# Kernel tuning notes

Hardware: AMD Instinct MI355X
Metric: run time of the kernel (lower is better)

## Reference

```python
import jax, jax.numpy as jnp
import numpy as np

D_MODEL = 1024
D_STATE = 16
D_CONV = 4
EXPAND = 2
D_INNER = EXPAND * D_MODEL          # 2048
DT_RANK = (D_MODEL + 15) // 16      # 64
B, L = 4, 2048


def setup_inputs() -> dict:
    key = jax.random.key(0)
    ks = jax.random.split(key, 10)
    s = 0.02
    x = jax.random.normal(ks[0], (B, L, D_MODEL), dtype=jnp.float32)
    # weights stored (in, out) so y = x @ W
    W_in = jax.random.normal(ks[1], (D_MODEL, 2 * D_INNER), dtype=jnp.float32) * s
    conv_w = jax.random.normal(ks[2], (D_INNER, D_CONV), dtype=jnp.float32) * 0.2
    conv_b = jnp.zeros((D_INNER,), dtype=jnp.float32)
    W_xproj = jax.random.normal(ks[3], (D_INNER, DT_RANK + 2 * D_STATE), dtype=jnp.float32) * s
    W_dt = jax.random.normal(ks[4], (DT_RANK, D_INNER), dtype=jnp.float32) * s
    b_dt = jax.random.uniform(ks[5], (D_INNER,), dtype=jnp.float32, minval=-4.0, maxval=-2.0)
    # S4D real init: A = -exp(A_log), A_log = log(1..d_state)
    A_log = jnp.log(jnp.broadcast_to(jnp.arange(1, D_STATE + 1, dtype=jnp.float32), (D_INNER, D_STATE)))
    Dp = jnp.ones((D_INNER,), dtype=jnp.float32)
    W_out = jax.random.normal(ks[6], (D_INNER, D_MODEL), dtype=jnp.float32) * s
    return {"x": x, "W_in": W_in, "conv_w": conv_w, "conv_b": conv_b,
            "W_xproj": W_xproj, "W_dt": W_dt, "b_dt": b_dt,
            "A_log": A_log, "Dp": Dp, "W_out": W_out}


def _causal_depthwise_conv(u, conv_w, conv_b):
    # u: (B, L, D_INNER); depthwise causal conv, kernel D_CONV
    uc = jnp.transpose(u, (0, 2, 1))                      # (B, D, L)
    k = conv_w[:, None, :]                                # (D, 1, K)
    y = jax.lax.conv_general_dilated(
        uc, k, window_strides=(1,), padding=[(D_CONV - 1, 0)],
        feature_group_count=D_INNER,
        dimension_numbers=('NCH', 'OIH', 'NCH'))
    y = y + conv_b[None, :, None]
    return jnp.transpose(y, (0, 2, 1))                    # (B, L, D)


def _selective_scan(u, delta, A, Bm, Cm, Dp):
    # u, delta: (B, L, d); A: (d, n); Bm, Cm: (B, L, n)
    def step(h, inp):
        u_t, dt_t, B_t, C_t = inp                         # (B,d),(B,d),(B,n),(B,n)
        dA = jnp.exp(dt_t[..., None] * A)                 # (B, d, n)
        h = h * dA + (dt_t * u_t)[..., None] * B_t[:, None, :]
        y = jnp.einsum('bdn,bn->bd', h, C_t)
        return h, y

    h0 = jnp.zeros((u.shape[0], u.shape[2], A.shape[1]), dtype=u.dtype)
    xs = (jnp.swapaxes(u, 0, 1), jnp.swapaxes(delta, 0, 1),
          jnp.swapaxes(Bm, 0, 1), jnp.swapaxes(Cm, 0, 1))
    _, ys = jax.lax.scan(step, h0, xs)
    y = jnp.swapaxes(ys, 0, 1)                            # (B, L, d)
    return y + u * Dp


def reference(x, W_in, conv_w, conv_b, W_xproj, W_dt, b_dt, A_log, Dp, W_out):
    xz = x @ W_in                                         # (B, L, 2*D_INNER)
    u, z = jnp.split(xz, 2, axis=-1)
    u = jax.nn.silu(_causal_depthwise_conv(u, conv_w, conv_b))
    proj = u @ W_xproj                                    # (B, L, DT_RANK + 2*D_STATE)
    dt_r = proj[..., :DT_RANK]
    Bm = proj[..., DT_RANK:DT_RANK + D_STATE]
    Cm = proj[..., DT_RANK + D_STATE:]
    delta = jax.nn.softplus(dt_r @ W_dt + b_dt)           # (B, L, D_INNER)
    A = -jnp.exp(A_log)                                   # (D_INNER, D_STATE)
    y = _selective_scan(u, delta, A, Bm, Cm, Dp)
    y = y * jax.nn.silu(z)
    return y @ W_out
```

## Files before the change

### kernel.cpp

```cpp
#include <hip/hip_runtime.h>
#include <hip/hip_bf16.h>
#include <math.h>

#define MTOK   8192
#define LSEQ   2048
#define NBATCH 4
#define DMODEL 1024
#define DINNER 2048
#define DSTATE 16
#define DTRANK 64
#define NXZ    4096
#define CHUNK  64
#define NCH    32
#define NPROJ  (MTOK * 96)
#define SPLITK 8

typedef _Float16 f16;
using f16x8 = __attribute__((ext_vector_type(8))) _Float16;
using f16x4 = __attribute__((ext_vector_type(4))) _Float16;
using f32x4 = __attribute__((ext_vector_type(4))) float;

__device__ __forceinline__ float silu_f(float x) { return x / (1.f + __expf(-x)); }

__device__ __forceinline__ void gload_lds16(const void* g, void* l) {
    __builtin_amdgcn_global_load_lds(
        (const __attribute__((address_space(1))) void*)g,
        (__attribute__((address_space(3))) void*)l, 16, 0, 0);
}

__global__ __launch_bounds__(256)
void cvt_f2h(const float* __restrict__ in, f16* __restrict__ out, int n4)
{
    const int i = blockIdx.x * 256 + threadIdx.x;
    if (i >= n4) return;
    const float4 v = ((const float4*)in)[i];
    f16x4 o;
    o[0] = (f16)v.x; o[1] = (f16)v.y; o[2] = (f16)v.z; o[3] = (f16)v.w;
    ((f16x4*)out)[i] = o;
}

__global__ __launch_bounds__(256)
void tcvt(const float* __restrict__ in, f16* __restrict__ out, int R, int C)
{
    __shared__ float t[32][33];
    const int c0 = blockIdx.x * 32, r0 = blockIdx.y * 32;
    const int tx = threadIdx.x & 31, ty = threadIdx.x >> 5;
    #pragma unroll
    for (int j = 0; j < 4; ++j)
        t[ty + 8 * j][tx] = in[(size_t)(r0 + ty + 8 * j) * C + c0 + tx];
    __syncthreads();
    #pragma unroll
    for (int j = 0; j < 4; ++j)
        out[(size_t)(c0 + ty + 8 * j) * R + r0 + tx] = (f16)t[tx][ty + 8 * j];
}

template<int EPI, typename OUT_T>
__global__ __launch_bounds__(256)
void hgemm128(const f16* __restrict__ A, int lda,
              const f16* __restrict__ Bt, int ldb,
              OUT_T* __restrict__ C, int ldc,
              int K, const float* __restrict__ bias,
              OUT_T* __restrict__ C2, int splitcol)
{
    __shared__ __align__(16) f16 As[2][128 * 32];
    __shared__ __align__(16) f16 Bs[2][128 * 32];

    const int tid  = threadIdx.x;
    const int lane = tid & 63, wave = tid >> 6;
    const int wr = wave >> 1, wc = wave & 1;
    const int row0 = blockIdx.x * 128;
    int col0 = blockIdx.y * 128;

    const int lrow = lane >> 2;
    const int lcol = ((lane & 3) ^ ((lane >> 3) & 3)) * 8;
    const f16* Agw = A  + (size_t)(row0 + wave * 32 + lrow) * lda + lcol;
    const f16* Bgw = Bt + (size_t)(col0 + wave * 32 + lrow) * ldb + lcol;
    const int ldsbase = (wave * 32) * 32;

    const int frow = lane & 15;
    const int fk   = (((lane >> 4) ^ ((frow >> 1) & 3))) * 8;
    const int nt = K / 32;

    f32x4 acc[4][4] = {};

    #pragma unroll
    for (int r = 0; r < 2; ++r) {
        gload_lds16(Agw + (size_t)r * 16 * lda, &As[0][ldsbase + r * 16 * 32]);
        gload_lds16(Bgw + (size_t)r * 16 * ldb, &Bs[0][ldsbase + r * 16 * 32]);
    }

    int cur = 0;
    for (int kt = 0; kt < nt; ++kt) {
        __syncthreads();
        if (kt + 1 < nt) {
            const int k0 = (kt + 1) * 32;
            #pragma unroll
            for (int r = 0; r < 2; ++r) {
                gload_lds16(Agw + (size_t)r * 16 * lda + k0, &As[cur ^ 1][ldsbase + r * 16 * 32]);
                gload_lds16(Bgw + (size_t)r * 16 * ldb + k0, &Bs[cur ^ 1][ldsbase + r * 16 * 32]);
            }
        }
        f16x8 af[4], bf[4];
        #pragma unroll
        for (int m = 0; m < 4; ++m)
            af[m] = *(const f16x8*)&As[cur][(wr * 64 + m * 16 + frow) * 32 + fk];
        #pragma unroll
        for (int n = 0; n < 4; ++n)
            bf[n] = *(const f16x8*)&Bs[cur][(wc * 64 + n * 16 + frow) * 32 + fk];
        #pragma unroll
        for (int m = 0; m < 4; ++m)
            #pragma unroll
            for (int n = 0; n < 4; ++n)
                acc[m][n] = __builtin_amdgcn_mfma_f32_16x16x32_f16(af[m], bf[n], acc[m][n], 0, 0, 0);
        cur ^= 1;
    }

    OUT_T* Cw = C;
    if (C2 != nullptr && col0 >= splitcol) { Cw = C2; col0 -= splitcol; }

    const int rbase = row0 + wr * 64 + (lane >> 4) * 4;
    const int cbase = col0 + wc * 64 + (lane & 15);
    #pragma unroll
    for (int m = 0; m < 4; ++m) {
        #pragma unroll
        for (int n = 0; n < 4; ++n) {
            const int col = cbase + n * 16;
            #pragma unroll
            for (int r = 0; r < 4; ++r) {
                const int row = rbase + m * 16 + r;
                float tv = acc[m][n][r];
                if (EPI == 1) {
                    tv += bias[col];
                    tv = (tv > 20.f) ? tv : __logf(1.f + __expf(tv));
                }
                Cw[(size_t)row * ldc + col] = (OUT_T)tv;
            }
        }
    }
}

__global__ __launch_bounds__(256)
void hgemm_n96(const f16* __restrict__ A,
               const f16* __restrict__ Bt,
               float* __restrict__ part)
{
    __shared__ __align__(16) f16 As[128][40];
    __shared__ __align__(16) f16 Bs[96][40];

    const int tid = threadIdx.x, lane = tid & 63, wave = tid >> 6;
    const int row0 = blockIdx.x * 128;
    const int sk = blockIdx.y;
    const int kbase = sk * (DINNER / SPLITK);

    const int srow = tid >> 1, skoff = (tid & 1) * 16;
    const f16* Ag = A  + (size_t)(row0 + srow) * DINNER + kbase + skoff;
    const f16* Bg = Bt + (size_t)srow * DINNER + kbase + skoff;

    const int frow = lane & 15, fk = (lane >> 4) * 8;

    f32x4 acc[2][6] = {};

    for (int kk = 0; kk < DINNER / SPLITK; kk += 32) {
        const f16x8 a0 = *(const f16x8*)(Ag + kk);
        const f16x8 a1 = *(const f16x8*)(Ag + kk + 8);
        f16x8 b0 = {}, b1 = {};
        if (tid < 192) { b0 = *(const f16x8*)(Bg + kk); b1 = *(const f16x8*)(Bg + kk + 8); }
        __syncthreads();
        *(f16x8*)&As[srow][skoff]     = a0;
        *(f16x8*)&As[srow][skoff + 8] = a1;
        if (tid < 192) {
            *(f16x8*)&Bs[srow][skoff]     = b0;
            *(f16x8*)&Bs[srow][skoff + 8] = b1;
        }
        __syncthreads();

        f16x8 af[2], bf[6];
        #pragma unroll
        for (int m = 0; m < 2; ++m)
            af[m] = *(const f16x8*)&As[wave * 32 + m * 16 + frow][fk];
        #pragma unroll
        for (int n = 0; n < 6; ++n)
            bf[n] = *(const f16x8*)&Bs[n * 16 + frow][fk];
        #pragma unroll
        for (int m = 0; m < 2; ++m)
            #pragma unroll
            for (int n = 0; n < 6; ++n)
                acc[m][n] = __builtin_amdgcn_mfma_f32_16x16x32_f16(af[m], bf[n], acc[m][n], 0, 0, 0);
    }

    #pragma unroll
    for (int m = 0; m < 2; ++m)
        #pragma unroll
        for (int n = 0; n < 6; ++n) {
            const int col = n * 16 + (lane & 15);
            #pragma unroll
            for (int r = 0; r < 4; ++r) {
                const int row = row0 + wave * 32 + m * 16 + (lane >> 4) * 4 + r;
                part[((size_t)sk * MTOK + row) * 96 + col] = acc[m][n][r];
            }
        }
}

__global__ __launch_bounds__(256)
void reduce3(const float* __restrict__ part, float* __restrict__ proj,
             f16* __restrict__ projh)
{
    const int e = blockIdx.x * 256 + threadIdx.x;
    float s = 0.f;
    #pragma unroll
    for (int i = 0; i < SPLITK; ++i) s += part[(size_t)i * NPROJ + e];
    proj[e]  = s;
    projh[e] = (f16)s;
}

__global__ __launch_bounds__(256)
void conv_silu_kernel(const f16* __restrict__ uph,
                      const float* __restrict__ cw, const float* __restrict__ cb,
                      f16* __restrict__ uh)
{
    const int mt  = blockIdx.x;
    const int ml0 = mt * 8;
    const int l0  = ml0 & (LSEQ - 1);
    const int d   = threadIdx.x * 8;

    float w[8][4];
    #pragma unroll
    for (int c = 0; c < 8; ++c) {
        const float4 wv = *(const float4*)(cw + (size_t)(d + c) * 4);
        w[c][0] = wv.x; w[c][1] = wv.y; w[c][2] = wv.z; w[c][3] = wv.w;
    }
    float bias[8];
    {
        const float4 b0 = *(const float4*)(cb + d);
        const float4 b1 = *(const float4*)(cb + d + 4);
        bias[0] = b0.x; bias[1] = b0.y; bias[2] = b0.z; bias[3] = b0.w;
        bias[4] = b1.x; bias[5] = b1.y; bias[6] = b1.z; bias[7] = b1.w;
    }

    f16x8 r[11];
    if (l0 != 0) {
        #pragma unroll
        for (int i = 0; i < 11; ++i)
            r[i] = *(const f16x8*)(uph + (size_t)(ml0 - 3 + i) * DINNER + d);
    } else {
        r[0] = f16x8{}; r[1] = f16x8{}; r[2] = f16x8{};
        #pragma unroll
        for (int i = 3; i < 11; ++i)
            r[i] = *(const f16x8*)(uph + (size_t)(ml0 - 3 + i) * DINNER + d);
    }

    #pragma unroll
    for (int i = 0; i < 8; ++i) {
        f16x8 o;
        #pragma unroll
        for (int c = 0; c < 8; ++c) {
            float a = bias[c];
            #pragma unroll
            for (int j = 0; j < 4; ++j)
                a = fmaf((float)r[i + j][c], w[c][j], a);
            o[c] = (f16)silu_f(a);
        }
        *(f16x8*)(uh + (size_t)(ml0 + i) * DINNER + d) = o;
    }
}

__device__ __forceinline__ bool load_A(const float* __restrict__ A_log, int d,
                                       float* Av)
{
    #pragma unroll
    for (int n = 0; n < DSTATE; ++n)
        Av[n] = -__expf(A_log[(size_t)d * DSTATE + n]);
    bool p = true;
    #pragma unroll
    for (int n = 1; n < DSTATE; ++n) {
        const float r = Av[n] / Av[0];
        if (fabsf(r - (float)(n + 1)) > 1e-3f) p = false;
    }
    return p;
}

__global__ __launch_bounds__(256)
void scan_pass1(const f16* __restrict__ uh,
                const f16* __restrict__ deltah,
                const float* __restrict__ proj,
                const float* __restrict__ A_log,
                float* __restrict__ Sbuf, float* __restrict__ sumdt)
{
    const int d = blockIdx.x * 256 + threadIdx.x;
    const int c = blockIdx.y;
    const int b = blockIdx.z;

    float Av[DSTATE];
    const bool pw = load_A(A_log, d, Av);
    const float Av0 = Av[0];

    const float* projb = proj + ((size_t)b * LSEQ + (size_t)c * CHUNK) * 96 + 64;

    float S[DSTATE];
    #pragma unroll
    for (int n = 0; n < DSTATE; ++n) S[n] = 0.f;
    float sdt = 0.f;

    const size_t tok0 = (size_t)b * LSEQ + (size_t)c * CHUNK;
    if (pw) {
        for (int l = 0; l < CHUNK; ++l) {
            const float* pr = projb + (size_t)l * 96;
            const float dt = (float)deltah[(tok0 + l) * DINNER + d];
            const float uu = (float)uh[(tok0 + l) * DINNER + d];
            sdt += dt;
            const float du = dt * uu;
            const float p1 = __expf(dt * Av0);
            const float p2 = p1 * p1;
            const float p3 = p2 * p1;
            const float p4 = p2 * p2;
            float m = 1.f;
            #pragma unroll
            for (int g = 0; g < 4; ++g) {
                const f32x4 bb = *(const f32x4*)(pr + g * 4);
                S[g*4+0] = fmaf(S[g*4+0], m * p1, du * bb[0]);
                S[g*4+1] = fmaf(S[g*4+1], m * p2, du * bb[1]);
                S[g*4+2] = fmaf(S[g*4+2], m * p3, du * bb[2]);
                S[g*4+3] = fmaf(S[g*4+3], m * p4, du * bb[3]);
                m *= p4;
            }
        }
    } else {
        for (int l = 0; l < CHUNK; ++l) {
            const float* pr = projb + (size_t)l * 96;
            const float dt = (float)deltah[(tok0 + l) * DINNER + d];
            const float uu = (float)uh[(tok0 + l) * DINNER + d];
            sdt += dt;
            const float du = dt * uu;
            #pragma unroll
            for (int n = 0; n < DSTATE; ++n)
                S[n] = fmaf(S[n], __expf(dt * Av[n]), du * pr[n]);
        }
    }

    const size_t base = (size_t)b * NCH + c;
    #pragma unroll
    for (int n = 0; n < DSTATE; ++n)
        Sbuf[(base * DSTATE + n) * DINNER + d] = S[n];
    sumdt[base * DINNER + d] = sdt;
}

__global__ __launch_bounds__(256)
void scan_pass2(const float* __restrict__ A_log,
                const float* __restrict__ sumdt,
                float* __restrict__ Sbuf)
{
    const int d = blockIdx.x * 256 + threadIdx.x;
    const int b = blockIdx.y;

    float Av[DSTATE];
    const bool pw = load_A(A_log, d, Av);
    const float Av0 = Av[0];

    float h[DSTATE];
    #pragma unroll
    for (int n = 0; n < DSTATE; ++n) h[n] = 0.f;

    for (int c = 0; c < NCH; ++c) {
        const size_t base = (size_t)b * NCH + c;
        const float sdt = sumdt[base * DINNER + d];
        if (pw) {
            const float p1 = __expf(sdt * Av0);
            const float p2 = p1 * p1;
            const float p3 = p2 * p1;
            const float p4 = p2 * p2;
            float m = 1.f;
            #pragma unroll
            for (int g = 0; g < 4; ++g) {
                const float pj[4] = {p1, p2, p3, p4};
                #pragma unroll
                for (int j = 0; j < 4; ++j) {
                    const int n = g * 4 + j;
                    const size_t idx = (base * DSTATE + n) * DINNER + d;
                    const float tmp = Sbuf[idx];
                    Sbuf[idx] = h[n];
                    h[n] = fmaf(h[n], m * pj[j], tmp);
                }
                m *= p4;
            }
        } else {
            #pragma unroll
            for (int n = 0; n < DSTATE; ++n) {
                const size_t idx = (base * DSTATE + n) * DINNER + d;
                const float tmp = Sbuf[idx];
                Sbuf[idx] = h[n];
                h[n] = fmaf(h[n], __expf(sdt * Av[n]), tmp);
            }
        }
    }
}

__global__ __launch_bounds__(256)
void scan_pass3(const f16* __restrict__ uh,
                const f16* __restrict__ deltah,
                const f16* __restrict__ zh,
                const float* __restrict__ proj,
                const float* __restrict__ A_log,
                const float* __restrict__ Dp,
                const float* __restrict__ Sbuf,
                f16* __restrict__ ygh)
{
    const int d = blockIdx.x * 256 + threadIdx.x;
    const int c = blockIdx.y;
    const int b = blockIdx.z;

    float Av[DSTATE];
    const bool pw = load_A(A_log, d, Av);
    const float Av0 = Av[0];

    float h[DSTATE];
    const size_t base = (size_t)b * NCH + c;
    #pragma unroll
    for (int n = 0; n < DSTATE; ++n)
        h[n] = Sbuf[(base * DSTATE + n) * DINNER + d];

    const float Dval = Dp[d];
    const float* projb = proj + ((size_t)b * LSEQ + (size_t)c * CHUNK) * 96 + 64;

    const size_t tok0 = (size_t)b * LSEQ + (size_t)c * CHUNK;
    for (int l = 0; l < CHUNK; ++l) {
        const float* pr = projb + (size_t)l * 96;
        const size_t tok = tok0 + l;
        const float dt = (float)deltah[tok * DINNER + d];
        const float uu = (float)uh[tok * DINNER + d];
        const float zz = (float)zh[tok * DINNER + d];
        const float du = dt * uu;
        float y = 0.f;
        if (pw) {
            const float p1 = __expf(dt * Av0);
            const float p2 = p1 * p1;
            const float p3 = p2 * p1;
            const float p4 = p2 * p2;
            float m = 1.f;
            #pragma unroll
            for (int g = 0; g < 4; ++g) {
                const f32x4 bb = *(const f32x4*)(pr + g * 4);
                const f32x4 cc = *(const f32x4*)(pr + 16 + g * 4);
                h[g*4+0] = fmaf(h[g*4+0], m * p1, du * bb[0]);
                h[g*4+1] = fmaf(h[g*4+1], m * p2, du * bb[1]);
                h[g*4+2] = fmaf(h[g*4+2], m * p3, du * bb[2]);
                h[g*4+3] = fmaf(h[g*4+3], m * p4, du * bb[3]);
                y = fmaf(h[g*4+0], cc[0], y);
                y = fmaf(h[g*4+1], cc[1], y);
                y = fmaf(h[g*4+2], cc[2], y);
                y = fmaf(h[g*4+3], cc[3], y);
                m *= p4;
            }
        } else {
            #pragma unroll
            for (int n = 0; n < DSTATE; ++n) {
                h[n] = fmaf(h[n], __expf(dt * Av[n]), du * pr[n]);
                y = fmaf(h[n], pr[16 + n], y);
            }
        }
        const float yt = fmaf(uu, Dval, y);
        ygh[tok * DINNER + d] = (f16)(yt * silu_f(zz));
    }
}

extern "C" void kernel_launch(void* const* d_in, const int* in_sizes, int n_in,
                              void* d_out, int out_size, void* d_ws, size_t ws_size,
                              hipStream_t stream)
{
    const float* x     = (const float*)d_in[0];
    const float* W_in  = (const float*)d_in[1];
    const float* cw    = (const float*)d_in[2];
    const float* cb    = (const float*)d_in[3];
    const float* W_xp  = (const float*)d_in[4];
    const float* W_dt  = (const float*)d_in[5];
    const float* b_dt  = (const float*)d_in[6];
    const float* A_log = (const float*)d_in[7];
    const float* Dp    = (const float*)d_in[8];
    const float* W_out = (const float*)d_in[9];
    float* out = (float*)d_out;

    float* updelta = (float*)d_ws;
    f16*   zh      = (f16*)(updelta + (size_t)MTOK * DINNER);
    f16*   uh      = zh + (size_t)MTOK * DINNER;
    float* proj    = (float*)(uh + (size_t)MTOK * DINNER);
    f16*   projh   = (f16*)(proj + NPROJ);
    float* Sbuf    = (float*)(projh + NPROJ);
    float* sumdt   = Sbuf + (size_t)NBATCH * NCH * DSTATE * DINNER;
    f16*   WxpT    = (f16*)(sumdt + (size_t)NBATCH * NCH * DINNER);
    f16*   WdtT    = WxpT + (size_t)96 * DINNER;
    f16*   WoutT   = WdtT + (size_t)DINNER * DTRANK;
    f16*   big     = WoutT + (size_t)DMODEL * DINNER;
    f16*   WinT    = big;
    float* part3   = (float*)(big + (size_t)NXZ * DMODEL);
    f16*   ygh     = big;
    f16*   xh      = uh;
    f16*   uph     = (f16*)updelta;
    f16*   deltah  = (f16*)updelta;

    cvt_f2h<<<(MTOK * DMODEL / 4 + 255) / 256, 256, 0, stream>>>(x, xh, MTOK * DMODEL / 4);
    tcvt<<<dim3(NXZ / 32, DMODEL / 32), 256, 0, stream>>>(W_in, WinT, DMODEL, NXZ);

    hgemm128<0, f16><<<dim3(64, 32), 256, 0, stream>>>(
        xh, DMODEL, WinT, DMODEL, uph, DINNER, DMODEL, nullptr, zh, DINNER);

    conv_silu_kernel<<<MTOK / 8, 256, 0, stream>>>(uph, cw, cb, uh);

    tcvt<<<dim3(96 / 32, DINNER / 32), 256, 0, stream>>>(W_xp, WxpT, DINNER, 96);
    hgemm_n96<<<dim3(64, SPLITK), 256, 0, stream>>>(uh, WxpT, part3);
    reduce3<<<NPROJ / 256, 256, 0, stream>>>(part3, proj, projh);

    tcvt<<<dim3(DINNER / 32, DTRANK / 32), 256, 0, stream>>>(W_dt, WdtT, DTRANK, DINNER);
    hgemm128<1, f16><<<dim3(64, 16), 256, 0, stream>>>(
        projh, 96, WdtT, DTRANK, deltah, DINNER, DTRANK, b_dt, nullptr, 0);

    scan_pass1<<<dim3(DINNER / 256, NCH, NBATCH), 256, 0, stream>>>(
        uh, deltah, proj, A_log, Sbuf, sumdt);
    scan_pass2<<<dim3(DINNER / 256, NBATCH), 256, 0, stream>>>(A_log, sumdt, Sbuf);
    scan_pass3<<<dim3(DINNER / 256, NCH, NBATCH), 256, 0, stream>>>(
        uh, deltah, zh, proj, A_log, Dp, Sbuf, ygh);

    tcvt<<<dim3(DMODEL / 32, DINNER / 32), 256, 0, stream>>>(W_out, WoutT, DINNER, DMODEL);
    hgemm128<0, float><<<dim3(64, 8), 256, 0, stream>>>(
        ygh, DINNER, WoutT, DINNER, out, DMODEL, DINNER, nullptr, nullptr, 0);
}
```

Baseline: 328.6 us.

## Replace in-projection GEMM with 256x256-tile, 8-wave pipelined MFMA kernel

Adds a new 512-thread GEMM with 256x256 output tiles, K-step 64, and swizzled LDS layout. Global-to-LDS loads are issued in half-tile pieces interleaved with the MFMA phases, with explicit waitcnt, barriers and setprio. It is used only for the large x@W_in projection. The goal is more data reuse per tile and better overlap of loads with compute. The cost is only 512 blocks at one block per CU and heavy register use from 32 accumulators per thread.

```diff
diff --git a/kernel.cpp b/kernel.cpp
--- a/kernel.cpp
+++ b/kernel.cpp
@@ -52,6 +52,115 @@
     #pragma unroll
     for (int j = 0; j < 4; ++j)
         out[(size_t)(c0 + ty + 8 * j) * R + r0 + tx] = (f16)t[tx][ty + 8 * j];
+}
+
+__global__ __launch_bounds__(512, 1)
+void hgemm256p(const f16* __restrict__ A, int lda,
+               const f16* __restrict__ Bt, int ldb,
+               f16* __restrict__ C, int ldc,
+               int K, f16* __restrict__ C2, int splitcol)
+{
+    __shared__ __align__(16) f16 SA[2][16384];
+    __shared__ __align__(16) f16 SB[2][16384];
+
+    const int tid  = threadIdx.x;
+    const int lane = tid & 63, w = tid >> 6;
+    const int wr = w >> 2, wc = w & 3;
+    const int row0 = blockIdx.x * 256;
+    int col0 = blockIdx.y * 256;
+
+    const int frow = lane & 15;
+    const int nt = K / 64;
+
+    auto issue_half = [&](int q) {
+        const int t = q >> 2, j = q & 3, buf = t & 1, k0 = t * 64;
+        const bool isA = (j >= 2);
+        const int hh = j & 1;
+        const f16* base = isA ? (A  + (size_t)(row0 + hh * 128) * lda + k0)
+                              : (Bt + (size_t)(col0 + hh * 128) * ldb + k0);
+        const int ld = isA ? lda : ldb;
+        f16* dst = (isA ? &SA[buf][0] : &SB[buf][0]) + hh * 8192;
+        #pragma unroll
+        for (int r2 = 0; r2 < 2; ++r2) {
+            const int ch = r2 * 512 + tid;
+            const int grow = ch >> 3;
+            const int gcol = (((ch & 7) * 16) ^ (((ch >> 5) & 1) << 5)) >> 1;
+            gload_lds16(base + (size_t)grow * ld + gcol, dst + ch * 8);
+        }
+    };
+
+    int next = 0;
+    for (; next < 6 && next < 4 * nt; ++next) issue_half(next);
+    asm volatile("s_waitcnt vmcnt(4)" ::: "memory");
+    asm volatile("s_barrier" ::: "memory");
+
+    f32x4 acc[8][4] = {};
+
+    for (int t = 0; t < nt; ++t) {
+        const int buf = t & 1;
+        const char* Ab = (const char*)&SA[buf][0];
+        const char* Bb = (const char*)&SB[buf][0];
+        f16x8 bf[4][2];
+        #pragma unroll
+        for (int p = 0; p < 4; ++p) {
+            f16x8 af[2][2];
+            if (p == 0) {
+                #pragma unroll
+                for (int n = 0; n < 4; ++n)
+                    #pragma unroll
+                    for (int ks = 0; ks < 2; ++ks) {
+                        const int R = wc * 64 + n * 16 + frow;
+                        const int off = R * 128 +
+                            ((ks * 64 + (lane >> 4) * 16) ^ (((R >> 2) & 1) << 5));
+                        bf[n][ks] = *(const f16x8*)(Bb + off);
+                    }
+            }
+            #pragma unroll
+            for (int i = 0; i < 2; ++i)
+                #pragma unroll
+                for (int ks = 0; ks < 2; ++ks) {
+                    const int R = wr * 128 + (2 * p + i) * 16 + frow;
+                    const int off = R * 128 +
+                        ((ks * 64 + (lane >> 4) * 16) ^ (((R >> 2) & 1) << 5));
+                    af[i][ks] = *(const f16x8*)(Ab + off);
+                }
+            if (next < 4 * nt) issue_half(next++);
+            asm volatile("s_barrier" ::: "memory");
+            asm volatile("s_waitcnt lgkmcnt(0)" ::: "memory");
+            __builtin_amdgcn_sched_barrier(0);
+            __builtin_amdgcn_s_setprio(1);
+            #pragma unroll
+            for (int i = 0; i < 2; ++i)
+                #pragma unroll
+                for (int n = 0; n < 4; ++n)
+                    #pragma unroll
+                    for (int ks = 0; ks < 2; ++ks)
+                        acc[2 * p + i][n] = __builtin_amdgcn_mfma_f32_16x16x32_f16(
+                            af[i][ks], bf[n][ks], acc[2 * p + i][n], 0, 0, 0);
+            __builtin_amdgcn_s_setprio(0);
+            if (p == 3 && t + 1 < nt) {
+                if (next >= 4 * t + 10) asm volatile("s_waitcnt vmcnt(4)" ::: "memory");
+                else                    asm volatile("s_waitcnt vmcnt(0)" ::: "memory");
+            }
+            asm volatile("s_barrier" ::: "memory");
+        }
+    }
+
+    f16* Cw = C;
+    if (C2 != nullptr && col0 >= splitcol) { Cw = C2; col0 -= splitcol; }
+
+    const int rbase = row0 + wr * 128 + (lane >> 4) * 4;
+    const int cbase = col0 + wc * 64 + (lane & 15);
+    #pragma unroll
+    for (int m = 0; m < 8; ++m) {
+        #pragma unroll
+        for (int n = 0; n < 4; ++n) {
+            const int col = cbase + n * 16;
+            #pragma unroll
+            for (int r = 0; r < 4; ++r)
+                Cw[(size_t)(rbase + m * 16 + r) * ldc + col] = (f16)acc[m][n][r];
+        }
+    }
 }
 
 template<int EPI, typename OUT_T>
@@ -499,8 +608,8 @@
     cvt_f2h<<<(MTOK * DMODEL / 4 + 255) / 256, 256, 0, stream>>>(x, xh, MTOK * DMODEL / 4);
     tcvt<<<dim3(NXZ / 32, DMODEL / 32), 256, 0, stream>>>(W_in, WinT, DMODEL, NXZ);
 
-    hgemm128<0, f16><<<dim3(64, 32), 256, 0, stream>>>(
-        xh, DMODEL, WinT, DMODEL, uph, DINNER, DMODEL, nullptr, zh, DINNER);
+    hgemm256p<<<dim3(32, 16), 512, 0, stream>>>(
+        xh, DMODEL, WinT, DMODEL, uph, DINNER, DMODEL, zh, DINNER);
 
     conv_silu_kernel<<<MTOK / 8, 256, 0, stream>>>(uph, cw, cb, uh);
 
```

Measured after the change: 319.3 us. -2.8%, faster.
